# Performance work log

Measured on AMD Instinct MI355X. Metric: run time of the kernel, lower is better.

## Reference

```python
import jax, jax.numpy as jnp
import numpy as np


def setup_inputs() -> dict:
    key = jax.random.key(0)
    k0, k1, k2, k3 = jax.random.split(key, 4)
    B, T, C, H = 8, 2048, 1024, 64
    x = jax.random.normal(k0, (B, T, C), dtype=jnp.float32)
    # nn.Linear(C, H, bias=False) weights, stored as (C, H) so y = x @ w
    w_q = jax.random.normal(k1, (C, H), dtype=jnp.float32) * (C ** -0.5)
    w_k = jax.random.normal(k2, (C, H), dtype=jnp.float32) * (C ** -0.5)
    w_v = jax.random.normal(k3, (C, H), dtype=jnp.float32) * (C ** -0.5)
    return {"x": x, "w_q": w_q, "w_k": w_k, "w_v": w_v}


def reference(x, w_q, w_k, w_v):
    # x: [B, T, C]; projections -> [B, T, H]
    B, T, C = x.shape
    q = jnp.einsum("btc,ch->bth", x, w_q)
    k = jnp.einsum("btc,ch->bth", x, w_k)
    v = jnp.einsum("btc,ch->bth", x, w_v)
    # NOTE: original scales by C**-0.5 (embedding dim), not head_size**-0.5
    scale = jnp.asarray(C, x.dtype) ** -0.5
    scores = jnp.einsum("bth,bsh->bts", q, k) * scale  # [B, T, T]
    causal = jnp.tril(jnp.ones((T, T), dtype=bool))
    scores = jnp.where(causal, scores, jnp.asarray(-jnp.inf, scores.dtype))
    attn = jax.nn.softmax(scores, axis=-1)
    # dropout is identity in eval / p=0
    return jnp.einsum("bts,bsh->bth", attn, v)
```

## Files before the change

kernel.cpp:

```cpp
#include <hip/hip_runtime.h>
#include <hip/hip_bf16.h>
#include <stdint.h>

#define TT 2048
#define CC 1024
#define HH 64

typedef __attribute__((ext_vector_type(8))) short short8;
typedef __attribute__((ext_vector_type(4))) short short4v;
typedef __attribute__((ext_vector_type(4))) float f32x4;
typedef __attribute__((ext_vector_type(2))) uint32_t u32x2;

static __device__ __forceinline__ short f2bf(float f) {
  union { float f; uint32_t u; } v; v.f = f;
  return (short)((v.u + 0x7fffu + ((v.u >> 16) & 1u)) >> 16);
}
static __device__ __forceinline__ uint32_t fbits(float f) {
  union { float f; uint32_t u; } v; v.f = f; return v.u;
}
static __device__ __forceinline__ uint32_t pk2t(float a, float b) {
  return __builtin_amdgcn_perm(fbits(b), fbits(a), 0x07060302);
}

#define MFMA(a, b, c) __builtin_amdgcn_mfma_f32_16x16x32_bf16((a), (b), (c), 0, 0, 0)

__global__ __launch_bounds__(256) void k_prep_wt(const float* __restrict__ wq,
                                                 const float* __restrict__ wk,
                                                 const float* __restrict__ wv,
                                                 short* __restrict__ wTf) {
  int t = blockIdx.x * 256 + threadIdx.x;
  int j    = t & 7;
  int lane = (t >> 3) & 63;
  int c32  = (t >> 9) & 31;
  int f    = t >> 14;
  int g = lane >> 4, tl = lane & 15;
  int m = f >> 2, n = f & 3;
  int c = c32 * 32 + 8 * g + j;
  int h = n * 16 + tl;
  const float* w = (m == 0) ? wq : (m == 1) ? wk : wv;
  float v = w[c * 64 + h];
  if (m == 0) v *= 0.03125f;
  wTf[t] = f2bf(v);
}

__global__ __launch_bounds__(512) void k_proj(const float* __restrict__ x,
                                              const short* __restrict__ wTf,
                                              short* __restrict__ q,
                                              short* __restrict__ k,
                                              short* __restrict__ vT) {
  __shared__ short xs[2048];
  int tid = threadIdx.x;
  int lane = tid & 63;
  int wave = tid >> 6;
  int g = lane >> 4, tl = lane & 15;
  int strip = wave >> 2, wn = wave & 3;
  int base = blockIdx.x * 32;

  int s_jh = tid & 1, s_g = (tid >> 1) & 3, s_kh = (tid >> 3) & 1,
      s_tl = (tid >> 4) & 15, s_st = (tid >> 8) & 1;
  const float* xg = x + (size_t)(base + s_st * 16 + s_tl) * CC + s_kh * 32 + 8 * s_g + 4 * s_jh;
  int fsw = s_kh * 4 + s_g;
  char* xw = (char*)xs + s_st * 2048 + s_kh * 1024 +
             (((s_g * 16 + s_tl) * 16) ^ (fsw << 4)) + s_jh * 8;
  const char* ra0 = (const char*)xs + strip * 2048 + ((lane * 16) ^ (g << 4));
  const char* ra1 = (const char*)xs + strip * 2048 + 1024 + ((lane * 16) ^ ((4 + g) << 4));

  f32x4 acc[3];
#pragma unroll
  for (int j3 = 0; j3 < 3; j3++) { acc[j3][0] = 0.f; acc[j3][1] = 0.f; acc[j3][2] = 0.f; acc[j3][3] = 0.f; }

  f32x4 pref = *(const f32x4*)xg;
  for (int step = 0; step < 16; ++step) {
    short4v wv4;
    wv4[0] = f2bf(pref[0]); wv4[1] = f2bf(pref[1]);
    wv4[2] = f2bf(pref[2]); wv4[3] = f2bf(pref[3]);
    if (step < 15) pref = *(const f32x4*)(xg + (step + 1) * 64);
    *(short4v*)xw = wv4;
    __syncthreads();
    short8 a0 = *(const short8*)ra0;
    short8 a1 = *(const short8*)ra1;
#pragma unroll
    for (int j3 = 0; j3 < 3; ++j3) {
      int f = wn * 3 + j3;
      const short* bp = wTf + f * 16384 + (step * 2) * 512 + lane * 8;
      short8 b0 = *(const short8*)bp;
      short8 b1 = *(const short8*)(bp + 512);
      acc[j3] = MFMA(a0, b0, acc[j3]);
      acc[j3] = MFMA(a1, b1, acc[j3]);
    }
    __syncthreads();
  }

  int trow = base + strip * 16 + 4 * g;
#pragma unroll
  for (int j3 = 0; j3 < 3; ++j3) {
    int f = wn * 3 + j3;
    int m = f >> 2, n = f & 3;
    if (m == 0) {
#pragma unroll
      for (int r = 0; r < 4; r++) q[(size_t)(trow + r) * HH + 16 * n + tl] = f2bf(acc[j3][r]);
    } else if (m == 1) {
#pragma unroll
      for (int r = 0; r < 4; r++) k[(size_t)(trow + r) * HH + 16 * n + tl] = f2bf(acc[j3][r]);
    } else {
      short4v pv;
      pv[0] = f2bf(acc[j3][0]); pv[1] = f2bf(acc[j3][1]);
      pv[2] = f2bf(acc[j3][2]); pv[3] = f2bf(acc[j3][3]);
      int bb = trow >> 11;
      int tloc = trow & 2047;
      *(short4v*)(vT + (size_t)bb * HH * TT + (size_t)(16 * n + tl) * TT + tloc) = pv;
    }
  }
}

__global__ __launch_bounds__(256) void k_attn(const short* __restrict__ q,
                                              const short* __restrict__ k,
                                              const short* __restrict__ vT,
                                              float* __restrict__ out) {
  __shared__ short plds[4][16][40];
  __shared__ float osh[4][64][17];
  __shared__ float lsh[4][16];
  int lane = threadIdx.x & 63;
  int wave = threadIdx.x >> 6;
  int g = lane >> 4, tl = lane & 15;
  int bid = blockIdx.x;
  int batch = bid >> 7;
  int i = bid & 127;
  int sub = (i & 1) ? (127 - (i >> 1)) : (i >> 1);
  int t0 = sub * 16;

  const short* qb = q + ((size_t)batch * TT + t0 + tl) * HH;
  const short* kb = k + (size_t)batch * TT * HH;
  const short* vb = vT + (size_t)batch * HH * TT;

  short8 qf0 = *(const short8*)(qb + 8 * g);
  short8 qf1 = *(const short8*)(qb + 32 + 8 * g);

  f32x4 o[4];
#pragma unroll
  for (int n = 0; n < 4; n++) { o[n][0] = 0.f; o[n][1] = 0.f; o[n][2] = 0.f; o[n][3] = 0.f; }
  float lrun = 0.f;
  int tq = t0 + tl;
  int nkt = (t0 >> 5) + 1;

  for (int kt = wave; kt < nkt - 1; kt += 4) {
    int s0 = kt * 32;
    const short* krow0 = kb + (size_t)(s0 + tl) * HH;
    const short* krow1 = kb + (size_t)(s0 + 16 + tl) * HH;
    short8 kf00 = *(const short8*)(krow0 + 8 * g);
    short8 kf01 = *(const short8*)(krow0 + 32 + 8 * g);
    short8 kf10 = *(const short8*)(krow1 + 8 * g);
    short8 kf11 = *(const short8*)(krow1 + 32 + 8 * g);
    short8 vf[4];
#pragma unroll
    for (int n = 0; n < 4; n++)
      vf[n] = *(const short8*)(vb + (size_t)(16 * n + tl) * TT + s0 + 8 * g);

    f32x4 z0; z0[0] = 0.f; z0[1] = 0.f; z0[2] = 0.f; z0[3] = 0.f;
    z0 = MFMA(kf00, qf0, z0);
    z0 = MFMA(kf01, qf1, z0);
    f32x4 z1; z1[0] = 0.f; z1[1] = 0.f; z1[2] = 0.f; z1[3] = 0.f;
    z1 = MFMA(kf10, qf0, z1);
    z1 = MFMA(kf11, qf1, z1);

    float p0 = __expf(z0[0] - 4.f), p1 = __expf(z0[1] - 4.f);
    float p2 = __expf(z0[2] - 4.f), p3 = __expf(z0[3] - 4.f);
    float p4 = __expf(z1[0] - 4.f), p5 = __expf(z1[1] - 4.f);
    float p6 = __expf(z1[2] - 4.f), p7 = __expf(z1[3] - 4.f);
    lrun += ((p0 + p1) + (p2 + p3)) + ((p4 + p5) + (p6 + p7));

    uint32_t* wrow = (uint32_t*)&plds[wave][tl][0];
    u32x2 w0; w0[0] = pk2t(p0, p1); w0[1] = pk2t(p2, p3);
    u32x2 w1; w1[0] = pk2t(p4, p5); w1[1] = pk2t(p6, p7);
    *(u32x2*)&wrow[2 * g] = w0;
    *(u32x2*)&wrow[8 + 2 * g] = w1;
    short8 pf = *(const short8*)&plds[wave][tl][8 * g];
#pragma unroll
    for (int n = 0; n < 4; n++) o[n] = MFMA(vf[n], pf, o[n]);
  }

  if (((nkt - 1) & 3) == wave) {
    int s0 = (nkt - 1) * 32;
    const short* krow0 = kb + (size_t)(s0 + tl) * HH;
    const short* krow1 = kb + (size_t)(s0 + 16 + tl) * HH;
    short8 kf00 = *(const short8*)(krow0 + 8 * g);
    short8 kf01 = *(const short8*)(krow0 + 32 + 8 * g);
    short8 kf10 = *(const short8*)(krow1 + 8 * g);
    short8 kf11 = *(const short8*)(krow1 + 32 + 8 * g);
    short8 vf[4];
#pragma unroll
    for (int n = 0; n < 4; n++)
      vf[n] = *(const short8*)(vb + (size_t)(16 * n + tl) * TT + s0 + 8 * g);

    f32x4 z0; z0[0] = 0.f; z0[1] = 0.f; z0[2] = 0.f; z0[3] = 0.f;
    z0 = MFMA(kf00, qf0, z0);
    z0 = MFMA(kf01, qf1, z0);
    f32x4 z1; z1[0] = 0.f; z1[1] = 0.f; z1[2] = 0.f; z1[3] = 0.f;
    z1 = MFMA(kf10, qf0, z1);
    z1 = MFMA(kf11, qf1, z1);

    float p[8];
#pragma unroll
    for (int st = 0; st < 2; ++st)
#pragma unroll
      for (int r = 0; r < 4; r++) {
        int sidx = s0 + st * 16 + 4 * g + r;
        float zz = (st == 0) ? z0[r] : z1[r];
        p[st * 4 + r] = (sidx <= tq) ? __expf(zz - 4.f) : 0.f;
      }
    lrun += ((p[0] + p[1]) + (p[2] + p[3])) + ((p[4] + p[5]) + (p[6] + p[7]));

    uint32_t* wrow = (uint32_t*)&plds[wave][tl][0];
    u32x2 w0; w0[0] = pk2t(p[0], p[1]); w0[1] = pk2t(p[2], p[3]);
    u32x2 w1; w1[0] = pk2t(p[4], p[5]); w1[1] = pk2t(p[6], p[7]);
    *(u32x2*)&wrow[2 * g] = w0;
    *(u32x2*)&wrow[8 + 2 * g] = w1;
    short8 pf = *(const short8*)&plds[wave][tl][8 * g];
#pragma unroll
    for (int n = 0; n < 4; n++) o[n] = MFMA(vf[n], pf, o[n]);
  }

  lrun += __shfl_xor(lrun, 16);
  lrun += __shfl_xor(lrun, 32);
#pragma unroll
  for (int n = 0; n < 4; n++)
#pragma unroll
    for (int r = 0; r < 4; r++) osh[wave][16 * n + 4 * g + r][tl] = o[n][r];
  if (lane < 16) lsh[wave][tl] = lrun;
  __syncthreads();

  int tid = threadIdx.x;
#pragma unroll
  for (int it = 0; it < 4; ++it) {
    int e = tid + 256 * it;
    int t = e >> 6, h = e & 63;
    float l = (lsh[0][t] + lsh[1][t]) + (lsh[2][t] + lsh[3][t]);
    float ov = (osh[0][h][t] + osh[1][h][t]) + (osh[2][h][t] + osh[3][h][t]);
    out[((size_t)batch * TT + t0 + t) * HH + h] = ov / l;
  }
}

extern "C" void kernel_launch(void* const* d_in, const int* in_sizes, int n_in,
                              void* d_out, int out_size, void* d_ws, size_t ws_size,
                              hipStream_t stream) {
  const float* x  = (const float*)d_in[0];
  const float* wq = (const float*)d_in[1];
  const float* wk = (const float*)d_in[2];
  const float* wv = (const float*)d_in[3];
  float* out = (float*)d_out;

  char* ws = (char*)d_ws;
  short* wTf = (short*)ws;
  short* q   = (short*)(ws + 393216);
  short* k   = (short*)(ws + 393216 + 2097152);
  short* vT  = (short*)(ws + 393216 + 2 * 2097152);

  k_prep_wt<<<768, 256, 0, stream>>>(wq, wk, wv, wTf);
  k_proj<<<512, 512, 0, stream>>>(x, wTf, q, k, vT);
  k_attn<<<1024, 256, 0, stream>>>(q, k, vT, out);
}
```

Baseline: 173.6 us.

## Pair complementary query tiles per attention block and double-buffer projection LDS

The attention kernel now handles two 16-row query tiles per block (tile p and tile 127-p) with 8 waves. Each K/V tile loaded is reused for both queries, which halves K/V global traffic and balances causal work across blocks. The projection kernel switches to a double-buffered, swizzled LDS tile covering 128 columns per step. That cuts the number of barrier steps from 16 to 8 and overlaps the global prefetch with the MFMAs. The cost is more registers per thread in attention (two accumulator sets) and a two-phase reduction epilogue with extra barriers.

```diff
diff --git a/kernel.cpp b/kernel.cpp
--- a/kernel.cpp
+++ b/kernel.cpp
@@ -48,7 +48,7 @@
                                               short* __restrict__ q,
                                               short* __restrict__ k,
                                               short* __restrict__ vT) {
-  __shared__ short xs[2048];
+  __shared__ short xls[2][32][128];
   int tid = threadIdx.x;
   int lane = tid & 63;
   int wave = tid >> 6;
@@ -56,37 +56,48 @@
   int strip = wave >> 2, wn = wave & 3;
   int base = blockIdx.x * 32;
 
-  int s_jh = tid & 1, s_g = (tid >> 1) & 3, s_kh = (tid >> 3) & 1,
-      s_tl = (tid >> 4) & 15, s_st = (tid >> 8) & 1;
-  const float* xg = x + (size_t)(base + s_st * 16 + s_tl) * CC + s_kh * 32 + 8 * s_g + 4 * s_jh;
-  int fsw = s_kh * 4 + s_g;
-  char* xw = (char*)xs + s_st * 2048 + s_kh * 1024 +
-             (((s_g * 16 + s_tl) * 16) ^ (fsw << 4)) + s_jh * 8;
-  const char* ra0 = (const char*)xs + strip * 2048 + ((lane * 16) ^ (g << 4));
-  const char* ra1 = (const char*)xs + strip * 2048 + 1024 + ((lane * 16) ^ ((4 + g) << 4));
+  int srow = tid >> 4, sslot = tid & 15;
+  const float* xg = x + (size_t)(base + srow) * CC + sslot * 8;
+  int woff = srow * 128 + ((sslot ^ (srow & 7)) << 3);
+  int rrow = strip * 16 + tl;
 
   f32x4 acc[3];
 #pragma unroll
   for (int j3 = 0; j3 < 3; j3++) { acc[j3][0] = 0.f; acc[j3][1] = 0.f; acc[j3][2] = 0.f; acc[j3][3] = 0.f; }
 
-  f32x4 pref = *(const f32x4*)xg;
-  for (int step = 0; step < 16; ++step) {
-    short4v wv4;
-    wv4[0] = f2bf(pref[0]); wv4[1] = f2bf(pref[1]);
-    wv4[2] = f2bf(pref[2]); wv4[3] = f2bf(pref[3]);
-    if (step < 15) pref = *(const f32x4*)(xg + (step + 1) * 64);
-    *(short4v*)xw = wv4;
-    __syncthreads();
-    short8 a0 = *(const short8*)ra0;
-    short8 a1 = *(const short8*)ra1;
-#pragma unroll
-    for (int j3 = 0; j3 < 3; ++j3) {
-      int f = wn * 3 + j3;
-      const short* bp = wTf + f * 16384 + (step * 2) * 512 + lane * 8;
-      short8 b0 = *(const short8*)bp;
-      short8 b1 = *(const short8*)(bp + 512);
-      acc[j3] = MFMA(a0, b0, acc[j3]);
-      acc[j3] = MFMA(a1, b1, acc[j3]);
+  f32x4 pa = *(const f32x4*)xg;
+  f32x4 pb = *(const f32x4*)(xg + 4);
+  {
+    short8 wv8;
+    wv8[0] = f2bf(pa[0]); wv8[1] = f2bf(pa[1]); wv8[2] = f2bf(pa[2]); wv8[3] = f2bf(pa[3]);
+    wv8[4] = f2bf(pb[0]); wv8[5] = f2bf(pb[1]); wv8[6] = f2bf(pb[2]); wv8[7] = f2bf(pb[3]);
+    *(short8*)(&xls[0][0][0] + woff) = wv8;
+  }
+  pa = *(const f32x4*)(xg + 128);
+  pb = *(const f32x4*)(xg + 132);
+  __syncthreads();
+
+  for (int step = 0; step < 8; ++step) {
+    const short* rb = &xls[step & 1][0][0];
+#pragma unroll
+    for (int kc = 0; kc < 4; ++kc) {
+      short8 a = *(const short8*)(rb + rrow * 128 + (((4 * kc + g) ^ (rrow & 7)) << 3));
+#pragma unroll
+      for (int j3 = 0; j3 < 3; ++j3) {
+        int f = wn * 3 + j3;
+        short8 b = *(const short8*)(wTf + f * 16384 + (step * 4 + kc) * 512 + lane * 8);
+        acc[j3] = MFMA(a, b, acc[j3]);
+      }
+    }
+    if (step < 7) {
+      short8 wv8;
+      wv8[0] = f2bf(pa[0]); wv8[1] = f2bf(pa[1]); wv8[2] = f2bf(pa[2]); wv8[3] = f2bf(pa[3]);
+      wv8[4] = f2bf(pb[0]); wv8[5] = f2bf(pb[1]); wv8[6] = f2bf(pb[2]); wv8[7] = f2bf(pb[3]);
+      *(short8*)(&xls[(step + 1) & 1][0][0] + woff) = wv8;
+      if (step < 6) {
+        pa = *(const f32x4*)(xg + (step + 2) * 128);
+        pb = *(const f32x4*)(xg + (step + 2) * 128 + 4);
+      }
     }
     __syncthreads();
   }
@@ -113,40 +124,85 @@
   }
 }
 
-__global__ __launch_bounds__(256) void k_attn(const short* __restrict__ q,
+static __device__ __forceinline__ void qtile_step(
+    short8 kf00, short8 kf01, short8 kf10, short8 kf11,
+    const short8 vf[4], short8 qf0, short8 qf1,
+    short* prow, int g, bool diag, int s0, int tq,
+    float& lrun, f32x4* o) {
+  f32x4 z0; z0[0] = 0.f; z0[1] = 0.f; z0[2] = 0.f; z0[3] = 0.f;
+  z0 = MFMA(kf00, qf0, z0);
+  z0 = MFMA(kf01, qf1, z0);
+  f32x4 z1; z1[0] = 0.f; z1[1] = 0.f; z1[2] = 0.f; z1[3] = 0.f;
+  z1 = MFMA(kf10, qf0, z1);
+  z1 = MFMA(kf11, qf1, z1);
+  float p[8];
+  if (diag) {
+#pragma unroll
+    for (int st = 0; st < 2; ++st)
+#pragma unroll
+      for (int r = 0; r < 4; ++r) {
+        int sidx = s0 + st * 16 + 4 * g + r;
+        float zz = (st == 0) ? z0[r] : z1[r];
+        p[st * 4 + r] = (sidx <= tq) ? __expf(zz - 4.f) : 0.f;
+      }
+  } else {
+#pragma unroll
+    for (int r = 0; r < 4; ++r) p[r] = __expf(z0[r] - 4.f);
+#pragma unroll
+    for (int r = 0; r < 4; ++r) p[4 + r] = __expf(z1[r] - 4.f);
+  }
+  lrun += ((p[0] + p[1]) + (p[2] + p[3])) + ((p[4] + p[5]) + (p[6] + p[7]));
+  uint32_t* wrow = (uint32_t*)prow;
+  u32x2 w0; w0[0] = pk2t(p[0], p[1]); w0[1] = pk2t(p[2], p[3]);
+  u32x2 w1; w1[0] = pk2t(p[4], p[5]); w1[1] = pk2t(p[6], p[7]);
+  *(u32x2*)&wrow[2 * g] = w0;
+  *(u32x2*)&wrow[8 + 2 * g] = w1;
+  short8 pf = *(const short8*)(prow + 8 * g);
+#pragma unroll
+  for (int n = 0; n < 4; ++n) o[n] = MFMA(vf[n], pf, o[n]);
+}
+
+__global__ __launch_bounds__(512) void k_attn(const short* __restrict__ q,
                                               const short* __restrict__ k,
                                               const short* __restrict__ vT,
                                               float* __restrict__ out) {
-  __shared__ short plds[4][16][40];
-  __shared__ float osh[4][64][17];
-  __shared__ float lsh[4][16];
-  int lane = threadIdx.x & 63;
-  int wave = threadIdx.x >> 6;
+  __shared__ float osh[8][64][17];
+  __shared__ float lsh[8][16];
+  __shared__ short plds[8][16][40];
+  int tid = threadIdx.x;
+  int lane = tid & 63;
+  int wave = tid >> 6;
   int g = lane >> 4, tl = lane & 15;
-  int bid = blockIdx.x;
-  int batch = bid >> 7;
-  int i = bid & 127;
-  int sub = (i & 1) ? (127 - (i >> 1)) : (i >> 1);
-  int t0 = sub * 16;
-
-  const short* qb = q + ((size_t)batch * TT + t0 + tl) * HH;
+  int batch = blockIdx.x >> 6;
+  int pid = blockIdx.x & 63;
+  int sa = pid, sb = 127 - pid;
+  int t0a = sa * 16, t0b = sb * 16;
+  int nkta = sa / 2 + 1, nktb = sb / 2 + 1;
+
   const short* kb = k + (size_t)batch * TT * HH;
   const short* vb = vT + (size_t)batch * HH * TT;
-
-  short8 qf0 = *(const short8*)(qb + 8 * g);
-  short8 qf1 = *(const short8*)(qb + 32 + 8 * g);
-
-  f32x4 o[4];
-#pragma unroll
-  for (int n = 0; n < 4; n++) { o[n][0] = 0.f; o[n][1] = 0.f; o[n][2] = 0.f; o[n][3] = 0.f; }
-  float lrun = 0.f;
-  int tq = t0 + tl;
-  int nkt = (t0 >> 5) + 1;
-
-  for (int kt = wave; kt < nkt - 1; kt += 4) {
+  const short* qa = q + ((size_t)batch * TT + t0a + tl) * HH;
+  const short* qbp = q + ((size_t)batch * TT + t0b + tl) * HH;
+
+  short8 qfA0 = *(const short8*)(qa + 8 * g);
+  short8 qfA1 = *(const short8*)(qa + 32 + 8 * g);
+  short8 qfB0 = *(const short8*)(qbp + 8 * g);
+  short8 qfB1 = *(const short8*)(qbp + 32 + 8 * g);
+
+  f32x4 oA[4], oB[4];
+#pragma unroll
+  for (int n = 0; n < 4; n++) {
+    oA[n][0] = 0.f; oA[n][1] = 0.f; oA[n][2] = 0.f; oA[n][3] = 0.f;
+    oB[n][0] = 0.f; oB[n][1] = 0.f; oB[n][2] = 0.f; oB[n][3] = 0.f;
+  }
+  float lA = 0.f, lB = 0.f;
+  int tqa = t0a + tl, tqb = t0b + tl;
+  short* prow = &plds[wave][tl][0];
+
+  for (int kt = wave; kt < nktb; kt += 8) {
     int s0 = kt * 32;
     const short* krow0 = kb + (size_t)(s0 + tl) * HH;
-    const short* krow1 = kb + (size_t)(s0 + 16 + tl) * HH;
+    const short* krow1 = krow0 + 16 * HH;
     short8 kf00 = *(const short8*)(krow0 + 8 * g);
     short8 kf01 = *(const short8*)(krow0 + 32 + 8 * g);
     short8 kf10 = *(const short8*)(krow1 + 8 * g);
@@ -156,87 +212,49 @@
     for (int n = 0; n < 4; n++)
       vf[n] = *(const short8*)(vb + (size_t)(16 * n + tl) * TT + s0 + 8 * g);
 
-    f32x4 z0; z0[0] = 0.f; z0[1] = 0.f; z0[2] = 0.f; z0[3] = 0.f;
-    z0 = MFMA(kf00, qf0, z0);
-    z0 = MFMA(kf01, qf1, z0);
-    f32x4 z1; z1[0] = 0.f; z1[1] = 0.f; z1[2] = 0.f; z1[3] = 0.f;
-    z1 = MFMA(kf10, qf0, z1);
-    z1 = MFMA(kf11, qf1, z1);
-
-    float p0 = __expf(z0[0] - 4.f), p1 = __expf(z0[1] - 4.f);
-    float p2 = __expf(z0[2] - 4.f), p3 = __expf(z0[3] - 4.f);
-    float p4 = __expf(z1[0] - 4.f), p5 = __expf(z1[1] - 4.f);
-    float p6 = __expf(z1[2] - 4.f), p7 = __expf(z1[3] - 4.f);
-    lrun += ((p0 + p1) + (p2 + p3)) + ((p4 + p5) + (p6 + p7));
-
-    uint32_t* wrow = (uint32_t*)&plds[wave][tl][0];
-    u32x2 w0; w0[0] = pk2t(p0, p1); w0[1] = pk2t(p2, p3);
-    u32x2 w1; w1[0] = pk2t(p4, p5); w1[1] = pk2t(p6, p7);
-    *(u32x2*)&wrow[2 * g] = w0;
-    *(u32x2*)&wrow[8 + 2 * g] = w1;
-    short8 pf = *(const short8*)&plds[wave][tl][8 * g];
-#pragma unroll
-    for (int n = 0; n < 4; n++) o[n] = MFMA(vf[n], pf, o[n]);
-  }
-
-  if (((nkt - 1) & 3) == wave) {
-    int s0 = (nkt - 1) * 32;
-    const short* krow0 = kb + (size_t)(s0 + tl) * HH;
-    const short* krow1 = kb + (size_t)(s0 + 16 + tl) * HH;
-    short8 kf00 = *(const short8*)(krow0 + 8 * g);
-    short8 kf01 = *(const short8*)(krow0 + 32 + 8 * g);
-    short8 kf10 = *(const short8*)(krow1 + 8 * g);
-    short8 kf11 = *(const short8*)(krow1 + 32 + 8 * g);
-    short8 vf[4];
-#pragma unroll
-    for (int n = 0; n < 4; n++)
-      vf[n] = *(const short8*)(vb + (size_t)(16 * n + tl) * TT + s0 + 8 * g);
-
-    f32x4 z0; z0[0] = 0.f; z0[1] = 0.f; z0[2] = 0.f; z0[3] = 0.f;
-    z0 = MFMA(kf00, qf0, z0);
-    z0 = MFMA(kf01, qf1, z0);
-    f32x4 z1; z1[0] = 0.f; z1[1] = 0.f; z1[2] = 0.f; z1[3] = 0.f;
-    z1 = MFMA(kf10, qf0, z1);
-    z1 = MFMA(kf11, qf1, z1);
-
-    float p[8];
-#pragma unroll
-    for (int st = 0; st < 2; ++st)
-#pragma unroll
-      for (int r = 0; r < 4; r++) {
-        int sidx = s0 + st * 16 + 4 * g + r;
-        float zz = (st == 0) ? z0[r] : z1[r];
-        p[st * 4 + r] = (sidx <= tq) ? __expf(zz - 4.f) : 0.f;
-      }
-    lrun += ((p[0] + p[1]) + (p[2] + p[3])) + ((p[4] + p[5]) + (p[6] + p[7]));
-
-    uint32_t* wrow = (uint32_t*)&plds[wave][tl][0];
-    u32x2 w0; w0[0] = pk2t(p[0], p[1]); w0[1] = pk2t(p[2], p[3]);
-    u32x2 w1; w1[0] = pk2t(p[4], p[5]); w1[1] = pk2t(p[6], p[7]);
-    *(u32x2*)&wrow[2 * g] = w0;
-    *(u32x2*)&wrow[8 + 2 * g] = w1;
-    short8 pf = *(const short8*)&plds[wave][tl][8 * g];
-#pragma unroll
-    for (int n = 0; n < 4; n++) o[n] = MFMA(vf[n], pf, o[n]);
-  }
-
-  lrun += __shfl_xor(lrun, 16);
-  lrun += __shfl_xor(lrun, 32);
+    qtile_step(kf00, kf01, kf10, kf11, vf, qfB0, qfB1, prow, g,
+               kt == nktb - 1, s0, tqb, lB, oB);
+    if (kt < nkta)
+      qtile_step(kf00, kf01, kf10, kf11, vf, qfA0, qfA1, prow, g,
+                 kt == nkta - 1, s0, tqa, lA, oA);
+  }
+
+  lA += __shfl_xor(lA, 16); lA += __shfl_xor(lA, 32);
+  lB += __shfl_xor(lB, 16); lB += __shfl_xor(lB, 32);
+
 #pragma unroll
   for (int n = 0; n < 4; n++)
 #pragma unroll
-    for (int r = 0; r < 4; r++) osh[wave][16 * n + 4 * g + r][tl] = o[n][r];
-  if (lane < 16) lsh[wave][tl] = lrun;
-  __syncthreads();
-
-  int tid = threadIdx.x;
-#pragma unroll
-  for (int it = 0; it < 4; ++it) {
-    int e = tid + 256 * it;
+    for (int r = 0; r < 4; r++) osh[wave][16 * n + 4 * g + r][tl] = oA[n][r];
+  if (lane < 16) lsh[wave][tl] = lA;
+  __syncthreads();
+#pragma unroll
+  for (int it = 0; it < 2; ++it) {
+    int e = tid + 512 * it;
     int t = e >> 6, h = e & 63;
-    float l = (lsh[0][t] + lsh[1][t]) + (lsh[2][t] + lsh[3][t]);
-    float ov = (osh[0][h][t] + osh[1][h][t]) + (osh[2][h][t] + osh[3][h][t]);
-    out[((size_t)batch * TT + t0 + t) * HH + h] = ov / l;
+    float l = ((lsh[0][t] + lsh[1][t]) + (lsh[2][t] + lsh[3][t])) +
+              ((lsh[4][t] + lsh[5][t]) + (lsh[6][t] + lsh[7][t]));
+    float ov = ((osh[0][h][t] + osh[1][h][t]) + (osh[2][h][t] + osh[3][h][t])) +
+               ((osh[4][h][t] + osh[5][h][t]) + (osh[6][h][t] + osh[7][h][t]));
+    out[((size_t)batch * TT + t0a + t) * HH + h] = ov / l;
+  }
+  __syncthreads();
+
+#pragma unroll
+  for (int n = 0; n < 4; n++)
+#pragma unroll
+    for (int r = 0; r < 4; r++) osh[wave][16 * n + 4 * g + r][tl] = oB[n][r];
+  if (lane < 16) lsh[wave][tl] = lB;
+  __syncthreads();
+#pragma unroll
+  for (int it = 0; it < 2; ++it) {
+    int e = tid + 512 * it;
+    int t = e >> 6, h = e & 63;
+    float l = ((lsh[0][t] + lsh[1][t]) + (lsh[2][t] + lsh[3][t])) +
+              ((lsh[4][t] + lsh[5][t]) + (lsh[6][t] + lsh[7][t]));
+    float ov = ((osh[0][h][t] + osh[1][h][t]) + (osh[2][h][t] + osh[3][h][t])) +
+               ((osh[4][h][t] + osh[5][h][t]) + (osh[6][h][t] + osh[7][h][t]));
+    out[((size_t)batch * TT + t0b + t) * HH + h] = ov / l;
   }
 }
 
@@ -257,5 +275,5 @@
 
   k_prep_wt<<<768, 256, 0, stream>>>(wq, wk, wv, wTf);
   k_proj<<<512, 512, 0, stream>>>(x, wTf, q, k, vT);
-  k_attn<<<1024, 256, 0, stream>>>(q, k, vT, out);
-}
+  k_attn<<<512, 512, 0, stream>>>(q, k, vT, out);
+}
```

New measurement: 144.3 us. -16.9%, faster.
